# Optimization experiments

Hardware: AMD Instinct MI355X
Metric: run time of the kernel (lower is better)

## Reference

```python
import jax, jax.numpy as jnp
import numpy as np

DT = 0.05
DX = 1.0
NUM_STEPS = 3
EPS = 1e-6
MAX_COEFF = 1.0  # use_implicit=True


def _thomas_const(r, d, eps):
    """Batched Thomas solve for the constant-coefficient system used by the ADI
    sweeps: off-diagonals a=c=-r, diagonal 1+2r with Neumann-like ends 1+r.
    Faithful to the torch solver including the +eps on b[0] and the
    clamp(min=eps) on interior denominators. d: (M, n) -> (M, n)."""
    n = d.shape[-1]
    a = -r  # scalar (lower == upper == -r)
    b = jnp.full((n,), 1.0 + 2.0 * r, dtype=d.dtype).at[0].set(1.0 + r).at[-1].set(1.0 + r)
    # forward elimination for c' and denominators (scalar per position)
    cp0 = a / (b[0] + eps)
    def fwd_c(cp_prev, bi):
        denom = jnp.maximum(bi - a * cp_prev, eps)
        cp = a / denom
        return cp, (cp, denom)
    _, (cps, denoms) = jax.lax.scan(fwd_c, cp0, b[1:])
    cp = jnp.concatenate([cp0[None], cps]).at[-1].set(0.0)  # (n,); last entry unused (torch leaves it 0)
    # forward sweep for d' over the whole batch of RHS vectors
    dT = jnp.moveaxis(d, -1, 0)  # (n, M)
    dp0 = dT[0] / (b[0] + eps)
    def fwd_d(dp_prev, xs):
        di, denom = xs
        dp = (di - a * dp_prev) / denom
        return dp, dp
    _, dps = jax.lax.scan(fwd_d, dp0, (dT[1:], denoms))
    dp = jnp.concatenate([dp0[None], dps], axis=0)  # (n, M)
    # back substitution
    xn = dp[-1]
    def back(x_next, xs):
        dpi, cpi = xs
        x = dpi - cpi * x_next
        return x, x
    _, xs_ = jax.lax.scan(back, xn, (dp[:-1], cp[:-1]), reverse=True)
    x = jnp.concatenate([xs_, xn[None]], axis=0)  # (n, M)
    return jnp.moveaxis(x, 0, -1)


def _forward(u, alpha_base, beta_base, alpha_spatial, beta_spatial, channel_coupling):
    B, C, H, W = u.shape
    # torch.einsum('cc,bci->bci', coupling, u) multiplies by the DIAGONAL of coupling
    diag = jnp.diagonal(channel_coupling)  # (C,)
    for step in range(NUM_STEPS):
        t = step * DT
        alpha_t = jnp.clip(alpha_base + alpha_spatial.mean(axis=(1, 2)) * t, EPS, MAX_COEFF)  # (C,)
        beta_t = jnp.clip(beta_base + beta_spatial.mean(axis=(1, 2)) * t, EPS, MAX_COEFF)
        r_a = alpha_t * (DT / 2.0) / DX ** 2  # ADI half-steps
        r_b = beta_t * (DT / 2.0) / DX ** 2
        uc = jnp.moveaxis(u, 1, 0)  # (C, B, H, W); coefficients differ per channel
        solve_x = lambda r, d: _thomas_const(r, d.reshape(B * H, W), EPS).reshape(B, H, W)
        ux = jax.vmap(solve_x)(r_a, uc)
        solve_y = lambda r, d: jnp.swapaxes(
            _thomas_const(r, jnp.swapaxes(d, 1, 2).reshape(B * W, H), EPS).reshape(B, W, H), 1, 2)
        uy = jax.vmap(solve_y)(r_b, ux)
        u = jnp.moveaxis(uy, 0, 1) * diag[None, :, None, None]
    return u


def setup_inputs() -> dict:
    key = jax.random.key(0)
    k = jax.random.split(key, 6)
    B, C, S = 128, 3, 256
    u = jax.random.normal(k[0], (B, C, S, S), dtype=jnp.float32)
    alpha_base = 0.3 + 0.01 * jax.random.normal(k[1], (C,), dtype=jnp.float32)
    beta_base = 0.3 + 0.01 * jax.random.normal(k[2], (C,), dtype=jnp.float32)
    alpha_spatial = 0.01 * jax.random.normal(k[3], (C, S, S), dtype=jnp.float32)
    beta_spatial = 0.01 * jax.random.normal(k[4], (C, S, S), dtype=jnp.float32)
    channel_coupling = 0.05 * jnp.eye(C, dtype=jnp.float32) + 0.01 * jax.random.normal(k[5], (C, C), dtype=jnp.float32)
    return {"u": u, "alpha_base": alpha_base, "beta_base": beta_base,
            "alpha_spatial": alpha_spatial, "beta_spatial": beta_spatial,
            "channel_coupling": channel_coupling}


def reference(u, alpha_base, beta_base, alpha_spatial, beta_spatial, channel_coupling):
    return _forward(u, alpha_base, beta_base, alpha_spatial, beta_spatial, channel_coupling)
```

## Files before the change

### kernel.cpp

```cpp
#include <hip/hip_runtime.h>

constexpr int Bn = 128, Cn = 3, Sn = 256;
constexpr int HWn = Sn * Sn;
constexpr int NPLANE = Bn * Cn;
constexpr float DTf = 0.05f;
constexpr float EPSf = 1e-6f;
constexpr float MAXCf = 1.0f;

#define WS_PART 32
#define WS_TAPX 128
#define WS_TAPY 10368

__global__ void means_part(const float* __restrict__ aspat,
                           const float* __restrict__ bspat,
                           float* __restrict__ ws) {
  int grp = blockIdx.x >> 4;
  int sub = blockIdx.x & 15;
  const float* base = (grp < 3) ? (aspat + grp * HWn) : (bspat + (grp - 3) * HWn);
  const float4* p = (const float4*)base + sub * 1024 + threadIdx.x;
  double acc = 0.0;
#pragma unroll
  for (int k = 0; k < 4; ++k) {
    float4 v = p[k * 256];
    acc += (double)v.x + (double)v.y + (double)v.z + (double)v.w;
  }
  __shared__ double sm[256];
  sm[threadIdx.x] = acc;
  __syncthreads();
  for (int s = 128; s > 0; s >>= 1) {
    if (threadIdx.x < s) sm[threadIdx.x] += sm[threadIdx.x + s];
    __syncthreads();
  }
  if (threadIdx.x == 0) ws[WS_PART + blockIdx.x] = (float)sm[0];
}

__global__ void build_taps(const float* __restrict__ alpha_base,
                           const float* __restrict__ beta_base,
                           const float* __restrict__ coupling,
                           float* __restrict__ ws) {
  __shared__ float cp3[3][288], di3[3][288];
  const int dirc = blockIdx.x, dir = dirc / 3, c = dirc % 3;
  const int j = threadIdx.x;
  if (j < 3) {
    const int k = j;
    double ms = 0.0;
    for (int m = 0; m < 16; ++m) ms += (double)ws[WS_PART + dirc * 16 + m];
    float mean = (float)(ms * (1.0 / 65536.0));
    float base = (dir == 0) ? alpha_base[c] : beta_base[c];
    float coef = fminf(fmaxf(base + mean * ((float)k * DTf), EPSf), MAXCf);
    float r = coef * (DTf * 0.5f);
    for (int p = 0; p < 16; ++p) {
      cp3[k][p] = 0.f; di3[k][p] = 0.f;
      cp3[k][272 + p] = 0.f; di3[k][272 + p] = 0.f;
    }
    float b0 = 1.f + r + EPSf;
    float cq = -r / b0, dq = 1.f / b0;
    cp3[k][16] = cq; di3[k][16] = dq;
    for (int i = 1; i < 256; ++i) {
      float b = (i == 255) ? (1.f + r) : (1.f + 2.f * r);
      float den = fmaxf(b + r * cq, EPSf);
      cq = -r / den; dq = 1.f / den;
      cp3[k][16 + i] = cq; di3[k][16 + i] = dq;
    }
  }
  float* tb = ws + ((dir == 0) ? WS_TAPX : WS_TAPY) + c * 13 * 256;
#pragma unroll
  for (int d = 0; d < 13; ++d) tb[d * 256 + j] = 0.f;
  __syncthreads();

  float z[33];
#pragma unroll
  for (int o = 0; o < 33; ++o) z[o] = (o == 16) ? 1.f : 0.f;
#pragma unroll
  for (int k = 0; k < 3; ++k) {
    float dp = 0.f;
#pragma unroll
    for (int o = 0; o < 33; ++o) {
      const int p = j + o;
      dp = fmaf(-cp3[k][p], dp, z[o] * di3[k][p]);
      z[o] = dp;
    }
    float x = 0.f;
#pragma unroll
    for (int o = 32; o >= 0; --o) {
      const int p = j + o;
      x = fmaf(-cp3[k][p], x, z[o]);
      z[o] = x;
    }
  }
  float scale = 1.f;
  if (dir == 1) {
    float dgc = coupling[c * 3 + c];
    scale = dgc * dgc * dgc;
  }
#pragma unroll
  for (int o = -6; o <= 6; ++o) {
    const int i = j + o;
    if ((unsigned)i < 256u) tb[(6 - o) * 256 + i] = z[o + 16] * scale;
  }
}

__global__ __launch_bounds__(512, 4) void conv3(
    const float* __restrict__ src, float* __restrict__ dst,
    const float* __restrict__ ws) {
  __shared__ float vt[76 * 256];
  const int t = threadIdx.x;
  const int logical = (blockIdx.x & 7) * 192 + (blockIdx.x >> 3);
  const int plane = logical >> 2;
  const int st = logical & 3;
  const int c = plane % 3;
  const int h0 = st * 64;
  const int a = (st == 0) ? 0 : (h0 - 6);
  const int b = (st == 3) ? 256 : (h0 + 70);
  const int Wv = b - a;
  const float* tpx = ws + WS_TAPX + c * 3328;
  const float* tpy = ws + WS_TAPY + c * 3328;
  float tx[13];
#pragma unroll
  for (int d = 0; d < 13; ++d) tx[d] = tpx[d * 256 + 128];
  const float* srcp = src + (size_t)plane * HWn;

  const int NU = 16 * Wv;
#pragma unroll
  for (int p = 0; p < 3; ++p) {
    const int u = t + 512 * p;
    if (u < NU) {
      const int s = u & 15, rl = u >> 4;
      const float* row = srcp + (size_t)(a + rl) * 256;
      float in_[32];
#pragma unroll
      for (int mq = 0; mq < 8; ++mq) {
        int cl = 16 * s - 8 + 4 * mq;
        cl = cl < 0 ? 0 : (cl > 252 ? 252 : cl);
        *(float4*)&in_[4 * mq] = *(const float4*)(row + cl);
      }
      float acc[16];
#pragma unroll
      for (int e = 0; e < 16; ++e) acc[e] = tx[0] * in_[e + 2];
#pragma unroll
      for (int d = 1; d < 13; ++d)
#pragma unroll
        for (int e = 0; e < 16; ++e) acc[e] = fmaf(tx[d], in_[e + 2 + d], acc[e]);
      if (s == 0) {
#pragma unroll
        for (int e = 0; e < 6; ++e) {
          float ac = 0.f;
#pragma unroll
          for (int d = 0; d < 13; ++d) ac = fmaf(tpx[d * 256 + e], in_[e + 2 + d], ac);
          acc[e] = ac;
        }
      } else if (s == 15) {
#pragma unroll
        for (int e = 10; e < 16; ++e) {
          float ac = 0.f;
#pragma unroll
          for (int d = 0; d < 13; ++d) ac = fmaf(tpx[d * 256 + 240 + e], in_[e + 2 + d], ac);
          acc[e] = ac;
        }
      }
      const int sw = rl & 7;
      float4* vr = (float4*)vt + rl * 64;
#pragma unroll
      for (int jj = 0; jj < 4; ++jj)
        vr[(4 * s + jj) ^ sw] =
            make_float4(acc[4 * jj], acc[4 * jj + 1], acc[4 * jj + 2], acc[4 * jj + 3]);
    }
  }
  __syncthreads();

  const int pr = t & 127, rc = t >> 7;
  const int jq = pr >> 1, jin = (pr & 1) * 2;
  const int g0 = h0 + 16 * rc;
  float2 win[13];
#pragma unroll
  for (int m = 0; m < 12; ++m) {
    int gg = g0 - 6 + m;
    gg = gg < a ? a : gg;
    const int rl = gg - a;
    win[m] = *(const float2*)(vt + rl * 256 + (((jq ^ (rl & 7)) << 2) | jin));
  }
  float* dstp = dst + (size_t)plane * HWn + 2 * pr;
#pragma unroll
  for (int rr = 0; rr < 16; ++rr) {
    const int g = g0 + rr;
    {
      int gg = g + 6;
      gg = gg > b - 1 ? b - 1 : gg;
      const int rl = gg - a;
      win[12] = *(const float2*)(vt + rl * 256 + (((jq ^ (rl & 7)) << 2) | jin));
    }
    const int gu = __builtin_amdgcn_readfirstlane(g);
    float ox, oy;
    {
      const float ty = tpy[gu];
      ox = ty * win[0].x; oy = ty * win[0].y;
    }
#pragma unroll
    for (int d = 1; d < 13; ++d) {
      const float ty = tpy[d * 256 + gu];
      ox = fmaf(ty, win[d].x, ox);
      oy = fmaf(ty, win[d].y, oy);
    }
    *(float2*)(dstp + (size_t)g * 256) = make_float2(ox, oy);
#pragma unroll
    for (int m = 0; m < 12; ++m) win[m] = win[m + 1];
  }
}

extern "C" void kernel_launch(void* const* d_in, const int* in_sizes, int n_in,
                              void* d_out, int out_size, void* d_ws, size_t ws_size,
                              hipStream_t stream) {
  const float* u = (const float*)d_in[0];
  const float* alpha_base = (const float*)d_in[1];
  const float* beta_base = (const float*)d_in[2];
  const float* alpha_spatial = (const float*)d_in[3];
  const float* beta_spatial = (const float*)d_in[4];
  const float* coupling = (const float*)d_in[5];
  float* out = (float*)d_out;
  float* ws = (float*)d_ws;

  means_part<<<96, 256, 0, stream>>>(alpha_spatial, beta_spatial, ws);
  build_taps<<<6, 256, 0, stream>>>(alpha_base, beta_base, coupling, ws);
  conv3<<<NPLANE * 4, 512, 0, stream>>>(u, out, ws);
}
```

Measured before the change: 89.74 us.

## Stage input rows into LDS via direct global-to-LDS loads and fuse mean reduction

The conv kernel now copies each tile's source rows straight into shared memory with global_load_lds (16-byte per lane, XOR-swizzled by column group) before the horizontal pass, then reads its inputs from LDS and writes the horizontal result back in place. The swizzle changes from row-based to column-based so the vertical pass indexes it with one fixed offset. The separate mean-reduction kernel is merged into build_taps, dropping a launch, but each of the 6 blocks now reduces a full 64K-element plane alone, which lengthens that serial stage.

```diff
diff --git a/kernel.cpp b/kernel.cpp
--- a/kernel.cpp
+++ b/kernel.cpp
@@ -7,48 +7,42 @@
 constexpr float EPSf = 1e-6f;
 constexpr float MAXCf = 1.0f;
 
-#define WS_PART 32
 #define WS_TAPX 128
 #define WS_TAPY 10368
 
-__global__ void means_part(const float* __restrict__ aspat,
-                           const float* __restrict__ bspat,
-                           float* __restrict__ ws) {
-  int grp = blockIdx.x >> 4;
-  int sub = blockIdx.x & 15;
-  const float* base = (grp < 3) ? (aspat + grp * HWn) : (bspat + (grp - 3) * HWn);
-  const float4* p = (const float4*)base + sub * 1024 + threadIdx.x;
-  double acc = 0.0;
-#pragma unroll
-  for (int k = 0; k < 4; ++k) {
-    float4 v = p[k * 256];
-    acc += (double)v.x + (double)v.y + (double)v.z + (double)v.w;
-  }
-  __shared__ double sm[256];
-  sm[threadIdx.x] = acc;
-  __syncthreads();
-  for (int s = 128; s > 0; s >>= 1) {
-    if (threadIdx.x < s) sm[threadIdx.x] += sm[threadIdx.x + s];
-    __syncthreads();
-  }
-  if (threadIdx.x == 0) ws[WS_PART + blockIdx.x] = (float)sm[0];
-}
-
 __global__ void build_taps(const float* __restrict__ alpha_base,
                            const float* __restrict__ beta_base,
+                           const float* __restrict__ aspat,
+                           const float* __restrict__ bspat,
                            const float* __restrict__ coupling,
                            float* __restrict__ ws) {
+  __shared__ double sm[256];
   __shared__ float cp3[3][288], di3[3][288];
+  __shared__ float s_mean;
   const int dirc = blockIdx.x, dir = dirc / 3, c = dirc % 3;
   const int j = threadIdx.x;
+  {
+    const float4* p = (const float4*)((dir == 0 ? aspat : bspat) + c * HWn) + j;
+    double acc = 0.0;
+#pragma unroll
+    for (int k2 = 0; k2 < 64; ++k2) {
+      float4 v = p[k2 * 256];
+      acc += (double)v.x + (double)v.y + (double)v.z + (double)v.w;
+    }
+    sm[j] = acc;
+    __syncthreads();
+    for (int s2 = 128; s2 > 0; s2 >>= 1) {
+      if (j < s2) sm[j] += sm[j + s2];
+      __syncthreads();
+    }
+    if (j == 0) s_mean = (float)(sm[0] * (1.0 / 65536.0));
+    __syncthreads();
+  }
   if (j < 3) {
     const int k = j;
-    double ms = 0.0;
-    for (int m = 0; m < 16; ++m) ms += (double)ws[WS_PART + dirc * 16 + m];
-    float mean = (float)(ms * (1.0 / 65536.0));
-    float base = (dir == 0) ? alpha_base[c] : beta_base[c];
-    float coef = fminf(fmaxf(base + mean * ((float)k * DTf), EPSf), MAXCf);
-    float r = coef * (DTf * 0.5f);
+    const float base = (dir == 0) ? alpha_base[c] : beta_base[c];
+    const float coef = fminf(fmaxf(base + s_mean * ((float)k * DTf), EPSf), MAXCf);
+    const float r = coef * (DTf * 0.5f);
     for (int p = 0; p < 16; ++p) {
       cp3[k][p] = 0.f; di3[k][p] = 0.f;
       cp3[k][272 + p] = 0.f; di3[k][272 + p] = 0.f;
@@ -115,10 +109,30 @@
   const int Wv = b - a;
   const float* tpx = ws + WS_TAPX + c * 3328;
   const float* tpy = ws + WS_TAPY + c * 3328;
+  const float* srcp = src + (size_t)plane * HWn;
+
+  {
+    const int wv = t >> 6, l = t & 63;
+    const int fl = l ^ (l >> 3);
+#pragma unroll
+    for (int m = 0; m < 3; ++m) {
+#pragma unroll
+      for (int jj = 0; jj < 4; ++jj) {
+        const int rl = 4 * wv + jj + 32 * m;
+        if (rl < Wv) {
+          const float* gp = srcp + (size_t)(a + rl) * 256 + (fl << 2);
+          __builtin_amdgcn_global_load_lds(
+              (const __attribute__((address_space(1))) void*)gp,
+              (__attribute__((address_space(3))) void*)(vt + rl * 256), 16, 0, 0);
+        }
+      }
+    }
+  }
   float tx[13];
 #pragma unroll
   for (int d = 0; d < 13; ++d) tx[d] = tpx[d * 256 + 128];
-  const float* srcp = src + (size_t)plane * HWn;
+  asm volatile("s_waitcnt vmcnt(0)" ::: "memory");
+  __builtin_amdgcn_sched_barrier(0);
 
   const int NU = 16 * Wv;
 #pragma unroll
@@ -126,13 +140,14 @@
     const int u = t + 512 * p;
     if (u < NU) {
       const int s = u & 15, rl = u >> 4;
-      const float* row = srcp + (size_t)(a + rl) * 256;
+      float* base = vt + rl * 256;
       float in_[32];
 #pragma unroll
       for (int mq = 0; mq < 8; ++mq) {
-        int cl = 16 * s - 8 + 4 * mq;
-        cl = cl < 0 ? 0 : (cl > 252 ? 252 : cl);
-        *(float4*)&in_[4 * mq] = *(const float4*)(row + cl);
+        int g = 4 * s - 2 + mq;
+        g = g < 0 ? 0 : (g > 63 ? 63 : g);
+        const int sl = g ^ (g >> 3);
+        *(float4*)&in_[4 * mq] = *(const float4*)(base + 4 * sl);
       }
       float acc[16];
 #pragma unroll
@@ -158,26 +173,27 @@
           acc[e] = ac;
         }
       }
-      const int sw = rl & 7;
-      float4* vr = (float4*)vt + rl * 64;
-#pragma unroll
-      for (int jj = 0; jj < 4; ++jj)
-        vr[(4 * s + jj) ^ sw] =
+#pragma unroll
+      for (int jj = 0; jj < 4; ++jj) {
+        const int q = 4 * s + jj;
+        const int sl = q ^ (q >> 3);
+        *(float4*)(base + 4 * sl) =
             make_float4(acc[4 * jj], acc[4 * jj + 1], acc[4 * jj + 2], acc[4 * jj + 3]);
+      }
     }
   }
   __syncthreads();
 
   const int pr = t & 127, rc = t >> 7;
-  const int jq = pr >> 1, jin = (pr & 1) * 2;
+  const int jq = pr >> 1;
+  const int wpos = ((jq ^ (jq >> 3)) << 2) | ((pr & 1) * 2);
   const int g0 = h0 + 16 * rc;
   float2 win[13];
 #pragma unroll
   for (int m = 0; m < 12; ++m) {
     int gg = g0 - 6 + m;
     gg = gg < a ? a : gg;
-    const int rl = gg - a;
-    win[m] = *(const float2*)(vt + rl * 256 + (((jq ^ (rl & 7)) << 2) | jin));
+    win[m] = *(const float2*)(vt + (gg - a) * 256 + wpos);
   }
   float* dstp = dst + (size_t)plane * HWn + 2 * pr;
 #pragma unroll
@@ -186,8 +202,7 @@
     {
       int gg = g + 6;
       gg = gg > b - 1 ? b - 1 : gg;
-      const int rl = gg - a;
-      win[12] = *(const float2*)(vt + rl * 256 + (((jq ^ (rl & 7)) << 2) | jin));
+      win[12] = *(const float2*)(vt + (gg - a) * 256 + wpos);
     }
     const int gu = __builtin_amdgcn_readfirstlane(g);
     float ox, oy;
@@ -219,7 +234,7 @@
   float* out = (float*)d_out;
   float* ws = (float*)d_ws;
 
-  means_part<<<96, 256, 0, stream>>>(alpha_spatial, beta_spatial, ws);
-  build_taps<<<6, 256, 0, stream>>>(alpha_base, beta_base, coupling, ws);
+  build_taps<<<6, 256, 0, stream>>>(alpha_base, beta_base,
+                                    alpha_spatial, beta_spatial, coupling, ws);
   conv3<<<NPLANE * 4, 512, 0, stream>>>(u, out, ws);
 }
```

Result: no change. 90.69 us (+1.1%).
